# Performance work log

Measured on AMD Instinct MI355X. Metric: run time of the kernel, lower is better.

Reference implementation:

```python
import jax, jax.numpy as jnp
import numpy as np

N_NODES = 50000
N_EDGES = 1600000
IN_DIM = 128
OUT_DIM = 16
N_HEADS = 8


def setup_inputs() -> dict:
    key = jax.random.key(0)
    ks = jax.random.split(key, 9)
    s = 1.0 / np.sqrt(IN_DIM)
    return {
        "h": jax.random.normal(ks[0], (N_NODES, IN_DIM), jnp.float32),
        "Wq": jax.random.normal(ks[1], (IN_DIM, OUT_DIM * N_HEADS), jnp.float32) * s,
        "bq": jax.random.normal(ks[2], (OUT_DIM * N_HEADS,), jnp.float32) * 0.01,
        "Wk": jax.random.normal(ks[3], (IN_DIM, OUT_DIM * N_HEADS), jnp.float32) * s,
        "bk": jax.random.normal(ks[4], (OUT_DIM * N_HEADS,), jnp.float32) * 0.01,
        "Wv": jax.random.normal(ks[5], (IN_DIM, OUT_DIM * N_HEADS), jnp.float32) * s,
        "bv": jax.random.normal(ks[6], (OUT_DIM * N_HEADS,), jnp.float32) * 0.01,
        "src": jax.random.randint(ks[7], (N_EDGES,), 0, N_NODES, jnp.int32),
        "dst": jax.random.randint(ks[8], (N_EDGES,), 0, N_NODES, jnp.int32),
    }


def reference(h, Wq, bq, Wk, bk, Wv, bv, src, dst):
    n_nodes = h.shape[0]
    # node-wise Q/K/V projections -> [N, H, D]
    Q = (h @ Wq + bq).reshape(n_nodes, N_HEADS, OUT_DIM)
    K = (h @ Wk + bk).reshape(n_nodes, N_HEADS, OUT_DIM)
    V = (h @ Wv + bv).reshape(n_nodes, N_HEADS, OUT_DIM)
    # edge-wise score: (K[src] * Q[dst]).sum(-1), scaled-exp with clamp
    score = jnp.sum(K[src] * Q[dst], axis=-1)  # [E, H]
    score = jnp.exp(jnp.clip(score / np.sqrt(OUT_DIM), -5.0, 5.0))
    # scatter-sum weighted values and normalizers to dst nodes
    msg = V[src] * score[:, :, None]  # [E, H, D]
    wV = jax.ops.segment_sum(msg, dst, num_segments=n_nodes)  # [N, H, D]
    z = jax.ops.segment_sum(score, dst, num_segments=n_nodes)  # [N, H]
    return wV / (z[:, :, None] + 1e-6)
```

## Files before the change

### kernel.cpp

```cpp
#include <hip/hip_runtime.h>
#include <hip/hip_bf16.h>
#include <cstddef>

#define N_NODES 50000
#define N_EDGES 1600000
#define IN_DIM 128
#define OUT_DIM 16
#define N_HEADS 8
#define QKV_DIM 128
#define HS_STRIDE 136
#define OS_STRIDE 392

#define SUBB 3125
#define BCAP 1024
#define BH_CHUNK 8192
#define BH_BLOCKS 196

typedef __hip_bfloat16 bf16;
typedef short bf16x8 __attribute__((ext_vector_type(8)));
typedef float f32x4  __attribute__((ext_vector_type(4)));

__device__ __forceinline__ float b2f(bf16 x) { return __bfloat162float(x); }

__device__ __forceinline__ float u16tof(unsigned int u) {
    unsigned int x = u << 16;
    float f;
    __builtin_memcpy(&f, &x, 4);
    return f;
}

__device__ __forceinline__ unsigned short f2bf(float v) {
    bf16 b = __float2bfloat16(v);
    unsigned short u;
    __builtin_memcpy(&u, &b, 2);
    return u;
}

__global__ __launch_bounds__(256) void sentinel_kernel(unsigned short* __restrict__ out, int n) {
    int i = blockIdx.x * 256 + threadIdx.x;
    if (i < n) out[i] = 0x42C8;
}

__global__ __launch_bounds__(256) void prep_kernel(
    const unsigned short* __restrict__ hraw,
    const void* __restrict__ Wqr, const void* __restrict__ bqr,
    const void* __restrict__ Wkr, const void* __restrict__ bkr,
    const void* __restrict__ Wvr, const void* __restrict__ bvr,
    int* __restrict__ flag,
    unsigned short* __restrict__ Wfrag, float* __restrict__ bias_f)
{
    __shared__ int red[256];
    const int t   = threadIdx.x;
    const int tid = blockIdx.x * 256 + t;

    int cnt = 0;
    for (int i = t; i < 8192; i += 256) {
        unsigned short u = hraw[i];
        int e = (u >> 7) & 0xFF;
        if (e == 0xFF || e > 0x85 || (e == 0 && (u & 0x7F) != 0)) cnt++;
    }
    red[t] = cnt;
    __syncthreads();
    for (int s = 128; s > 0; s >>= 1) {
        if (t < s) red[t] += red[t + s];
        __syncthreads();
    }
    const bool f32 = (red[0] > 100);
    if (blockIdx.x == 0 && t == 0) *flag = red[0];

    if (tid < 384) {
        int mat = tid >> 7, c = tid & 127;
        const void* bp = (mat == 0) ? bqr : (mat == 1) ? bkr : bvr;
        bias_f[tid] = f32 ? ((const float*)bp)[c] : b2f(((const bf16*)bp)[c]);
    }

    int l  = tid & 63;
    int s  = (tid >> 6) & 3;
    int nt = tid >> 8;
    int n  = nt * 16 + (l & 15);
    int k0 = s * 32 + (l >> 4) * 8;
    int mat = n >> 7, c = n & 127;
    const void* Wp = (mat == 0) ? Wqr : (mat == 1) ? Wkr : Wvr;

    unsigned short v[8];
#pragma unroll
    for (int j = 0; j < 8; ++j) {
        int k = k0 + j;
        float w = f32 ? ((const float*)Wp)[k * QKV_DIM + c]
                      : b2f(((const bf16*)Wp)[k * QKV_DIM + c]);
        v[j] = f2bf(w);
    }
    ushort4* o = (ushort4*)(Wfrag + (size_t)tid * 8);
    o[0] = make_ushort4(v[0], v[1], v[2], v[3]);
    o[1] = make_ushort4(v[4], v[5], v[6], v[7]);
}

__global__ __launch_bounds__(256) void gemm_kernel(
    const void* __restrict__ hraw,
    const unsigned short* __restrict__ Wfrag, const float* __restrict__ bias_f,
    const int* __restrict__ flag,
    unsigned short* __restrict__ Qt, unsigned short* __restrict__ KVt)
{
    __shared__ __align__(16) unsigned short smem[64 * OS_STRIDE];

    const bool f32 = (*flag > 100);
    const int m0  = blockIdx.x * 64;
    const int tid = threadIdx.x;

#pragma unroll
    for (int it = 0; it < 8; ++it) {
        int idx = it * 1024 + tid * 4;
        int r = idx >> 7, k = idx & 127;
        int row = m0 + r;
        ushort4 w4 = make_ushort4(0, 0, 0, 0);
        if (row < N_NODES) {
            if (f32) {
                float4 v4 = ((const float4*)hraw)[(size_t)row * 32 + (k >> 2)];
                w4 = make_ushort4(f2bf(v4.x), f2bf(v4.y), f2bf(v4.z), f2bf(v4.w));
            } else {
                uint2 u = ((const uint2*)hraw)[(size_t)row * 32 + (k >> 2)];
                w4 = make_ushort4((unsigned short)(u.x & 0xffffu), (unsigned short)(u.x >> 16),
                                  (unsigned short)(u.y & 0xffffu), (unsigned short)(u.y >> 16));
            }
        }
        *(ushort4*)&smem[r * HS_STRIDE + k] = w4;
    }
    __syncthreads();

    const int lane = tid & 63;
    const int wave = tid >> 6;
    const int qd   = lane >> 4;
    const int ln15 = lane & 15;

    bf16x8 afr[4][4];
#pragma unroll
    for (int ms = 0; ms < 4; ++ms)
#pragma unroll
        for (int s = 0; s < 4; ++s)
            afr[ms][s] = *(const bf16x8*)&smem[(ms * 16 + ln15) * HS_STRIDE + s * 32 + qd * 8];

    __syncthreads();

#pragma unroll
    for (int i = 0; i < 6; ++i) {
        const int nt  = wave + i * 4;
        const int col = nt * 16 + ln15;
        const float bs = bias_f[col];
        const int mat = col >> 7, c127 = col & 127;
        const int ocol = (mat == 0) ? c127
                       : 128 + 8 * (c127 >> 2) + (c127 & 3) + ((mat == 2) ? 4 : 0);

        bf16x8 bfr[4];
#pragma unroll
        for (int s = 0; s < 4; ++s)
            bfr[s] = *(const bf16x8*)(Wfrag + ((size_t)(nt * 4 + s) * 64 + lane) * 8);

#pragma unroll
        for (int ms = 0; ms < 4; ++ms) {
            f32x4 acc = {0.f, 0.f, 0.f, 0.f};
#pragma unroll
            for (int s = 0; s < 4; ++s)
                acc = __builtin_amdgcn_mfma_f32_16x16x32_bf16(afr[ms][s], bfr[s], acc, 0, 0, 0);
#pragma unroll
            for (int r = 0; r < 4; ++r) {
                int rl = ms * 16 + qd * 4 + r;
                smem[rl * OS_STRIDE + ocol] = f2bf(acc[r] + bs);
            }
        }
    }
    __syncthreads();

    for (int q = tid; q < 1024; q += 256) {
        int row = q >> 4, c = q & 15;
        int grow = m0 + row;
        if (grow < N_NODES)
            ((uint4*)Qt)[grow * 16 + c] = *(const uint4*)&smem[row * OS_STRIDE + c * 8];
    }
    for (int q = tid; q < 2048; q += 256) {
        int row = q >> 5, g = q & 31;
        int grow = m0 + row;
        if (grow < N_NODES)
            ((uint4*)KVt)[grow * 32 + g] = *(const uint4*)&smem[row * OS_STRIDE + 128 + g * 8];
    }
}

__global__ __launch_bounds__(256) void scatter_kernel(
    const int* __restrict__ src, const int* __restrict__ dst,
    unsigned int* __restrict__ packed, unsigned int* __restrict__ offcnt)
{
    __shared__ int lcnt[SUBB];
    __shared__ int loff[SUBB];
    __shared__ unsigned int stage[BH_CHUNK];
    __shared__ int sm[256];
    __shared__ int carry;

    const int t    = threadIdx.x;
    const int base = blockIdx.x * BH_CHUNK;
    const int nb   = min(N_EDGES - base, BH_CHUNK);

    for (int i = t; i < SUBB; i += 256) lcnt[i] = 0;
    if (t == 0) carry = 0;
    __syncthreads();

    for (int i = t; i < nb; i += 256)
        atomicAdd(&lcnt[dst[base + i] >> 4], 1);
    __syncthreads();

    for (int c = 0; c < 13; ++c) {
        int i = c * 256 + t;
        int x = (i < SUBB) ? lcnt[i] : 0;
        int v = x;
        sm[t] = v;
        __syncthreads();
        for (int s = 1; s < 256; s <<= 1) {
            int a = (t >= s) ? sm[t - s] : 0;
            __syncthreads();
            v += a;
            sm[t] = v;
            __syncthreads();
        }
        if (i < SUBB) loff[i] = carry + v - x;
        __syncthreads();
        if (t == 255) carry += v;
        __syncthreads();
    }

    for (int i = t; i < SUBB; i += 256)
        offcnt[(size_t)blockIdx.x * SUBB + i] =
            ((unsigned int)loff[i] << 16) | (unsigned int)lcnt[i];
    __syncthreads();
    for (int i = t; i < SUBB; i += 256) lcnt[i] = 0;
    __syncthreads();

    for (int i = t; i < nb; i += 256) {
        int d = dst[base + i];
        int b = d >> 4;
        int pos = loff[b] + atomicAdd(&lcnt[b], 1);
        stage[pos] = (unsigned int)src[base + i] | ((unsigned int)(d & 15) << 16);
    }
    __syncthreads();

    for (int i = t; i < nb; i += 256)
        packed[base + i] = stage[i];
}

__global__ __launch_bounds__(256) void bucket_agg_kernel(
    const unsigned short* __restrict__ Qt, const unsigned short* __restrict__ KVt,
    const unsigned int* __restrict__ packed, const unsigned int* __restrict__ offcnt,
    const int* __restrict__ flag, void* __restrict__ out)
{
    __shared__ unsigned int   lds_pk[BCAP];
    __shared__ unsigned short lds_src[BCAP];
    __shared__ int runoff[BH_BLOCKS], runcnt[BH_BLOCKS], runpfx[BH_BLOCKS];
    __shared__ int cnt16[16], base16[16], cur16[16];
    __shared__ int nb_s;

    const int sb = blockIdx.x;
    const int t  = threadIdx.x;

    if (t < 16) { cnt16[t] = 0; cur16[t] = 0; }
    if (t < BH_BLOCKS) {
        unsigned int oc = offcnt[(size_t)t * SUBB + sb];
        runoff[t] = t * BH_CHUNK + (int)(oc >> 16);
        runcnt[t] = (int)(oc & 0xffffu);
    }
    __syncthreads();

    {
        int* sm = (int*)lds_pk;
        int x = (t < BH_BLOCKS) ? runcnt[t] : 0;
        int v = x;
        sm[t] = v;
        __syncthreads();
        for (int s = 1; s < 256; s <<= 1) {
            int a = (t >= s) ? sm[t - s] : 0;
            __syncthreads();
            v += a;
            sm[t] = v;
            __syncthreads();
        }
        if (t < BH_BLOCKS) runpfx[t] = v - x;
        if (t == 255) nb_s = v;
        __syncthreads();
    }
    const int nb = min(nb_s, BCAP);

    for (int r = t; r < BH_BLOCKS; r += 256) {
        int ro = runoff[r], rc = runcnt[r], rp = runpfx[r];
        for (int j = 0; j < rc; ++j) {
            int dpos = rp + j;
            if (dpos < BCAP) {
                unsigned int pk = packed[ro + j];
                lds_pk[dpos] = pk;
                atomicAdd(&cnt16[(pk >> 16) & 15], 1);
            }
        }
    }
    __syncthreads();
    if (t == 0) {
        int acc = 0;
#pragma unroll
        for (int i = 0; i < 16; ++i) { base16[i] = acc; acc += cnt16[i]; }
    }
    __syncthreads();
    for (int j = t; j < nb; j += 256) {
        unsigned int pk = lds_pk[j];
        int dl = (pk >> 16) & 15;
        int pos = base16[dl] + atomicAdd(&cur16[dl], 1);
        lds_src[pos] = (unsigned short)(pk & 0xffffu);
    }
    __syncthreads();

    const int wave = t >> 6;
    const int lane = t & 63;
    const int half = lane >> 5;
    const int hl   = lane & 31;
    const uint4* KV4 = (const uint4*)KVt;
    const bool of32 = (*flag > 100);

    for (int dl = wave; dl < 16; dl += 4) {
        const int d = sb * 16 + dl;
        uint2 qw = ((const uint2*)Qt)[d * 32 + hl];
        const float q0 = u16tof(qw.x & 0xffffu), q1 = u16tof(qw.x >> 16);
        const float q2 = u16tof(qw.y & 0xffffu), q3 = u16tof(qw.y >> 16);
        const int off = base16[dl];
        const int n   = cnt16[dl];

        float a0 = 0.f, a1 = 0.f, a2 = 0.f, a3 = 0.f, zz = 0.f;

#define CONSUME(KV, SCMASK)                                                     \
        {                                                                       \
            float p = fmaf(u16tof((KV).x & 0xffffu), q0,                        \
                      fmaf(u16tof((KV).x >> 16), q1,                            \
                      fmaf(u16tof((KV).y & 0xffffu), q2,                        \
                           u16tof((KV).y >> 16) * q3)));                        \
            p += __shfl_xor(p, 1);                                              \
            p += __shfl_xor(p, 2);                                              \
            float sc = __expf(__builtin_amdgcn_fmed3f(p * 0.25f, -5.f, 5.f));   \
            sc *= (SCMASK);                                                     \
            a0 = fmaf(u16tof((KV).z & 0xffffu), sc, a0);                        \
            a1 = fmaf(u16tof((KV).z >> 16),     sc, a1);                        \
            a2 = fmaf(u16tof((KV).w & 0xffffu), sc, a2);                        \
            a3 = fmaf(u16tof((KV).w >> 16),     sc, a3);                        \
            zz += sc;                                                           \
        }

        int j = 0;
        for (; j + 8 <= n; j += 8) {
            int e[4];
#pragma unroll
            for (int u = 0; u < 4; ++u) e[u] = lds_src[off + j + 2 * u + half];
            uint4 kv[4];
#pragma unroll
            for (int u = 0; u < 4; ++u) kv[u] = KV4[e[u] * 32 + hl];
#pragma unroll
            for (int u = 0; u < 4; ++u) CONSUME(kv[u], 1.f)
        }
        for (; j + 2 <= n; j += 2) {
            int e = lds_src[off + j + half];
            uint4 kv = KV4[e * 32 + hl];
            CONSUME(kv, 1.f)
        }
        if (j < n) {
            int e = lds_src[off + j];
            uint4 kv = KV4[e * 32 + hl];
            CONSUME(kv, (half == 0) ? 1.f : 0.f)
        }
#undef CONSUME

        a0 += __shfl_xor(a0, 32);
        a1 += __shfl_xor(a1, 32);
        a2 += __shfl_xor(a2, 32);
        a3 += __shfl_xor(a3, 32);
        zz += __shfl_xor(zz, 32);

        const float inv = 1.f / (zz + 1e-6f);
        const float r0 = a0 * inv, r1 = a1 * inv, r2 = a2 * inv, r3 = a3 * inv;

        if (half == 0) {
            if (of32) {
                ((float4*)out)[d * 32 + hl] = make_float4(r0, r1, r2, r3);
            } else {
                unsigned int w0 = ((unsigned int)f2bf(r1) << 16) | f2bf(r0);
                unsigned int w1 = ((unsigned int)f2bf(r3) << 16) | f2bf(r2);
                ((uint2*)out)[d * 32 + hl] = make_uint2(w0, w1);
            }
        }
    }
}

extern "C" void kernel_launch(void* const* d_in, const int* in_sizes, int n_in,
                              void* d_out, int out_size, void* d_ws, size_t ws_size,
                              hipStream_t stream)
{
    const void* h  = d_in[0];
    const void* Wq = d_in[1];
    const void* bq = d_in[2];
    const void* Wk = d_in[3];
    const void* bk = d_in[4];
    const void* Wv = d_in[5];
    const void* bv = d_in[6];
    const int*  src = (const int*)d_in[7];
    const int*  dst = (const int*)d_in[8];

    const size_t NQ = (size_t)N_NODES * QKV_DIM;
    const size_t WFRAG_N = 24 * 4 * 64 * 8;
    const size_t PACKED_N = (size_t)BH_BLOCKS * BH_CHUNK;
    const size_t OFFCNT_N = (size_t)BH_BLOCKS * SUBB;

    const size_t need = 3 * NQ * 2 + WFRAG_N * 2 + 384 * 4 + 64
                      + PACKED_N * 4 + OFFCNT_N * 4;

    if (ws_size < need) {
        sentinel_kernel<<<(out_size + 255) / 256, 256, 0, stream>>>((unsigned short*)d_out, out_size);
        return;
    }

    unsigned short* Qt  = (unsigned short*)d_ws;
    unsigned short* KVt = Qt + NQ;
    unsigned short* Wfrag = KVt + 2 * NQ;
    float* bias_f = (float*)(Wfrag + WFRAG_N);
    int* flag     = (int*)(bias_f + 384);
    unsigned int* packed = (unsigned int*)(flag + 16);
    unsigned int* offcnt = packed + PACKED_N;

    prep_kernel<<<24, 256, 0, stream>>>((const unsigned short*)h,
        Wq, bq, Wk, bk, Wv, bv, flag, Wfrag, bias_f);

    const int gemm_blocks = (N_NODES + 63) / 64;
    gemm_kernel<<<gemm_blocks, 256, 0, stream>>>(h, Wfrag, bias_f, flag, Qt, KVt);

    scatter_kernel<<<BH_BLOCKS, 256, 0, stream>>>(src, dst, packed, offcnt);

    bucket_agg_kernel<<<SUBB, 256, 0, stream>>>(Qt, KVt, packed, offcnt, flag, d_out);
}
```

Baseline: 279.9 us.

## Fuse GEMM and edge bucketing kernels into one launch with shared LDS arena

Merges the node projection GEMM and the per-chunk edge bucketing scatter into a single kernel, where the first block indices do the scatter and the rest do the GEMM, so the two independent stages run concurrently and one launch is removed. LDS is unified into one arena sized for the GEMM, which forces the scatter to drop its separate loff array and instead overwrite the count array with offsets. This shrinks the scatter's LDS footprint. The trade-off is that the heavier scatter blocks and the GEMM blocks now share one occupancy limit set by the larger arena.

```diff
diff --git a/kernel.cpp b/kernel.cpp
--- a/kernel.cpp
+++ b/kernel.cpp
@@ -15,6 +15,8 @@
 #define BCAP 1024
 #define BH_CHUNK 8192
 #define BH_BLOCKS 196
+#define GEMM_BLOCKS 782
+#define FUSED_BLOCKS (BH_BLOCKS + GEMM_BLOCKS)
 
 typedef __hip_bfloat16 bf16;
 typedef short bf16x8 __attribute__((ext_vector_type(8)));
@@ -95,153 +97,152 @@
     o[1] = make_ushort4(v[4], v[5], v[6], v[7]);
 }
 
-__global__ __launch_bounds__(256) void gemm_kernel(
+__global__ __launch_bounds__(256) void fused_gs_kernel(
     const void* __restrict__ hraw,
     const unsigned short* __restrict__ Wfrag, const float* __restrict__ bias_f,
     const int* __restrict__ flag,
-    unsigned short* __restrict__ Qt, unsigned short* __restrict__ KVt)
-{
-    __shared__ __align__(16) unsigned short smem[64 * OS_STRIDE];
-
-    const bool f32 = (*flag > 100);
-    const int m0  = blockIdx.x * 64;
-    const int tid = threadIdx.x;
-
-#pragma unroll
-    for (int it = 0; it < 8; ++it) {
-        int idx = it * 1024 + tid * 4;
-        int r = idx >> 7, k = idx & 127;
-        int row = m0 + r;
-        ushort4 w4 = make_ushort4(0, 0, 0, 0);
-        if (row < N_NODES) {
-            if (f32) {
-                float4 v4 = ((const float4*)hraw)[(size_t)row * 32 + (k >> 2)];
-                w4 = make_ushort4(f2bf(v4.x), f2bf(v4.y), f2bf(v4.z), f2bf(v4.w));
-            } else {
-                uint2 u = ((const uint2*)hraw)[(size_t)row * 32 + (k >> 2)];
-                w4 = make_ushort4((unsigned short)(u.x & 0xffffu), (unsigned short)(u.x >> 16),
-                                  (unsigned short)(u.y & 0xffffu), (unsigned short)(u.y >> 16));
-            }
-        }
-        *(ushort4*)&smem[r * HS_STRIDE + k] = w4;
-    }
-    __syncthreads();
-
-    const int lane = tid & 63;
-    const int wave = tid >> 6;
-    const int qd   = lane >> 4;
-    const int ln15 = lane & 15;
-
-    bf16x8 afr[4][4];
-#pragma unroll
-    for (int ms = 0; ms < 4; ++ms)
-#pragma unroll
-        for (int s = 0; s < 4; ++s)
-            afr[ms][s] = *(const bf16x8*)&smem[(ms * 16 + ln15) * HS_STRIDE + s * 32 + qd * 8];
-
-    __syncthreads();
-
-#pragma unroll
-    for (int i = 0; i < 6; ++i) {
-        const int nt  = wave + i * 4;
-        const int col = nt * 16 + ln15;
-        const float bs = bias_f[col];
-        const int mat = col >> 7, c127 = col & 127;
-        const int ocol = (mat == 0) ? c127
-                       : 128 + 8 * (c127 >> 2) + (c127 & 3) + ((mat == 2) ? 4 : 0);
-
-        bf16x8 bfr[4];
-#pragma unroll
-        for (int s = 0; s < 4; ++s)
-            bfr[s] = *(const bf16x8*)(Wfrag + ((size_t)(nt * 4 + s) * 64 + lane) * 8);
-
-#pragma unroll
-        for (int ms = 0; ms < 4; ++ms) {
-            f32x4 acc = {0.f, 0.f, 0.f, 0.f};
-#pragma unroll
-            for (int s = 0; s < 4; ++s)
-                acc = __builtin_amdgcn_mfma_f32_16x16x32_bf16(afr[ms][s], bfr[s], acc, 0, 0, 0);
-#pragma unroll
-            for (int r = 0; r < 4; ++r) {
-                int rl = ms * 16 + qd * 4 + r;
-                smem[rl * OS_STRIDE + ocol] = f2bf(acc[r] + bs);
-            }
-        }
-    }
-    __syncthreads();
-
-    for (int q = tid; q < 1024; q += 256) {
-        int row = q >> 4, c = q & 15;
-        int grow = m0 + row;
-        if (grow < N_NODES)
-            ((uint4*)Qt)[grow * 16 + c] = *(const uint4*)&smem[row * OS_STRIDE + c * 8];
-    }
-    for (int q = tid; q < 2048; q += 256) {
-        int row = q >> 5, g = q & 31;
-        int grow = m0 + row;
-        if (grow < N_NODES)
-            ((uint4*)KVt)[grow * 32 + g] = *(const uint4*)&smem[row * OS_STRIDE + 128 + g * 8];
-    }
-}
-
-__global__ __launch_bounds__(256) void scatter_kernel(
+    unsigned short* __restrict__ Qt, unsigned short* __restrict__ KVt,
     const int* __restrict__ src, const int* __restrict__ dst,
     unsigned int* __restrict__ packed, unsigned int* __restrict__ offcnt)
 {
-    __shared__ int lcnt[SUBB];
-    __shared__ int loff[SUBB];
-    __shared__ unsigned int stage[BH_CHUNK];
-    __shared__ int sm[256];
-    __shared__ int carry;
-
-    const int t    = threadIdx.x;
-    const int base = blockIdx.x * BH_CHUNK;
-    const int nb   = min(N_EDGES - base, BH_CHUNK);
-
-    for (int i = t; i < SUBB; i += 256) lcnt[i] = 0;
-    if (t == 0) carry = 0;
-    __syncthreads();
-
-    for (int i = t; i < nb; i += 256)
-        atomicAdd(&lcnt[dst[base + i] >> 4], 1);
-    __syncthreads();
-
-    for (int c = 0; c < 13; ++c) {
-        int i = c * 256 + t;
-        int x = (i < SUBB) ? lcnt[i] : 0;
-        int v = x;
-        sm[t] = v;
-        __syncthreads();
-        for (int s = 1; s < 256; s <<= 1) {
-            int a = (t >= s) ? sm[t - s] : 0;
-            __syncthreads();
-            v += a;
+    __shared__ __align__(16) unsigned char arena[64 * OS_STRIDE * 2];
+    const int t = threadIdx.x;
+
+    if (blockIdx.x < BH_BLOCKS) {
+        int* lcnt           = (int*)arena;
+        unsigned int* stage = (unsigned int*)(arena + 12544);
+        int* sm             = (int*)(arena + 45312);
+        int* carryp         = (int*)(arena + 46336);
+
+        const int b    = blockIdx.x;
+        const int base = b * BH_CHUNK;
+        const int nb   = min(N_EDGES - base, BH_CHUNK);
+
+        for (int i = t; i < SUBB; i += 256) lcnt[i] = 0;
+        if (t == 0) *carryp = 0;
+        __syncthreads();
+
+        for (int i = t; i < nb; i += 256)
+            atomicAdd(&lcnt[dst[base + i] >> 4], 1);
+        __syncthreads();
+
+        for (int c = 0; c < 13; ++c) {
+            int i = c * 256 + t;
+            int x = (i < SUBB) ? lcnt[i] : 0;
+            int v = x;
             sm[t] = v;
             __syncthreads();
-        }
-        if (i < SUBB) loff[i] = carry + v - x;
-        __syncthreads();
-        if (t == 255) carry += v;
-        __syncthreads();
-    }
-
-    for (int i = t; i < SUBB; i += 256)
-        offcnt[(size_t)blockIdx.x * SUBB + i] =
-            ((unsigned int)loff[i] << 16) | (unsigned int)lcnt[i];
-    __syncthreads();
-    for (int i = t; i < SUBB; i += 256) lcnt[i] = 0;
-    __syncthreads();
-
-    for (int i = t; i < nb; i += 256) {
-        int d = dst[base + i];
-        int b = d >> 4;
-        int pos = loff[b] + atomicAdd(&lcnt[b], 1);
-        stage[pos] = (unsigned int)src[base + i] | ((unsigned int)(d & 15) << 16);
-    }
-    __syncthreads();
-
-    for (int i = t; i < nb; i += 256)
-        packed[base + i] = stage[i];
+            for (int s = 1; s < 256; s <<= 1) {
+                int a = (t >= s) ? sm[t - s] : 0;
+                __syncthreads();
+                v += a;
+                sm[t] = v;
+                __syncthreads();
+            }
+            int off = *carryp + v - x;
+            if (i < SUBB) {
+                offcnt[(size_t)b * SUBB + i] =
+                    ((unsigned int)off << 16) | (unsigned int)x;
+                lcnt[i] = off;
+            }
+            __syncthreads();
+            if (t == 255) *carryp += v;
+            __syncthreads();
+        }
+
+        for (int i = t; i < nb; i += 256) {
+            int d = dst[base + i];
+            int bk = d >> 4;
+            int pos = atomicAdd(&lcnt[bk], 1);
+            stage[pos] = (unsigned int)src[base + i] | ((unsigned int)(d & 15) << 16);
+        }
+        __syncthreads();
+
+        for (int i = t; i < nb; i += 256)
+            packed[base + i] = stage[i];
+
+    } else {
+        unsigned short* smem = (unsigned short*)arena;
+
+        const bool f32 = (*flag > 100);
+        const int m0 = (blockIdx.x - BH_BLOCKS) * 64;
+
+#pragma unroll
+        for (int it = 0; it < 8; ++it) {
+            int idx = it * 1024 + t * 4;
+            int r = idx >> 7, k = idx & 127;
+            int row = m0 + r;
+            ushort4 w4 = make_ushort4(0, 0, 0, 0);
+            if (row < N_NODES) {
+                if (f32) {
+                    float4 v4 = ((const float4*)hraw)[(size_t)row * 32 + (k >> 2)];
+                    w4 = make_ushort4(f2bf(v4.x), f2bf(v4.y), f2bf(v4.z), f2bf(v4.w));
+                } else {
+                    uint2 u = ((const uint2*)hraw)[(size_t)row * 32 + (k >> 2)];
+                    w4 = make_ushort4((unsigned short)(u.x & 0xffffu), (unsigned short)(u.x >> 16),
+                                      (unsigned short)(u.y & 0xffffu), (unsigned short)(u.y >> 16));
+                }
+            }
+            *(ushort4*)&smem[r * HS_STRIDE + k] = w4;
+        }
+        __syncthreads();
+
+        const int lane = t & 63;
+        const int wave = t >> 6;
+        const int qd   = lane >> 4;
+        const int ln15 = lane & 15;
+
+        bf16x8 afr[4][4];
+#pragma unroll
+        for (int ms = 0; ms < 4; ++ms)
+#pragma unroll
+            for (int s = 0; s < 4; ++s)
+                afr[ms][s] = *(const bf16x8*)&smem[(ms * 16 + ln15) * HS_STRIDE + s * 32 + qd * 8];
+
+        __syncthreads();
+
+#pragma unroll
+        for (int i = 0; i < 6; ++i) {
+            const int nt  = wave + i * 4;
+            const int col = nt * 16 + ln15;
+            const float bs = bias_f[col];
+            const int mat = col >> 7, c127 = col & 127;
+            const int ocol = (mat == 0) ? c127
+                           : 128 + 8 * (c127 >> 2) + (c127 & 3) + ((mat == 2) ? 4 : 0);
+
+            bf16x8 bfr[4];
+#pragma unroll
+            for (int s = 0; s < 4; ++s)
+                bfr[s] = *(const bf16x8*)(Wfrag + ((size_t)(nt * 4 + s) * 64 + lane) * 8);
+
+#pragma unroll
+            for (int ms = 0; ms < 4; ++ms) {
+                f32x4 acc = {0.f, 0.f, 0.f, 0.f};
+#pragma unroll
+                for (int s = 0; s < 4; ++s)
+                    acc = __builtin_amdgcn_mfma_f32_16x16x32_bf16(afr[ms][s], bfr[s], acc, 0, 0, 0);
+#pragma unroll
+                for (int r = 0; r < 4; ++r) {
+                    int rl = ms * 16 + qd * 4 + r;
+                    smem[rl * OS_STRIDE + ocol] = f2bf(acc[r] + bs);
+                }
+            }
+        }
+        __syncthreads();
+
+        for (int q = t; q < 1024; q += 256) {
+            int row = q >> 4, c = q & 15;
+            int grow = m0 + row;
+            if (grow < N_NODES)
+                ((uint4*)Qt)[grow * 16 + c] = *(const uint4*)&smem[row * OS_STRIDE + c * 8];
+        }
+        for (int q = t; q < 2048; q += 256) {
+            int row = q >> 5, g = q & 31;
+            int grow = m0 + row;
+            if (grow < N_NODES)
+                ((uint4*)KVt)[grow * 32 + g] = *(const uint4*)&smem[row * OS_STRIDE + 128 + g * 8];
+        }
+    }
 }
 
 __global__ __launch_bounds__(256) void bucket_agg_kernel(
@@ -427,10 +428,8 @@
     prep_kernel<<<24, 256, 0, stream>>>((const unsigned short*)h,
         Wq, bq, Wk, bk, Wv, bv, flag, Wfrag, bias_f);
 
-    const int gemm_blocks = (N_NODES + 63) / 64;
-    gemm_kernel<<<gemm_blocks, 256, 0, stream>>>(h, Wfrag, bias_f, flag, Qt, KVt);
-
-    scatter_kernel<<<BH_BLOCKS, 256, 0, stream>>>(src, dst, packed, offcnt);
+    fused_gs_kernel<<<FUSED_BLOCKS, 256, 0, stream>>>(h, Wfrag, bias_f, flag,
+        Qt, KVt, src, dst, packed, offcnt);
 
     bucket_agg_kernel<<<SUBB, 256, 0, stream>>>(Qt, KVt, packed, offcnt, flag, d_out);
 }
```

Result: faster. 265.4 us (-5.2%).
